# Optimization experiments

Hardware: AMD Instinct MI355X
Metric: run time of the kernel (lower is better)

## Reference

```python
import jax, jax.numpy as jnp
import numpy as np

H = 16  # num_heads

def setup_inputs() -> dict:
    key = jax.random.key(0)
    k1, k2, k3 = jax.random.split(key, 3)
    D = 1024
    x = jax.random.normal(k1, (4, 2048, D), dtype=jnp.float32)
    W_qkv = jax.random.normal(k2, (D, 3 * D), dtype=jnp.float32) * (1.0 / np.sqrt(D))
    b_qkv = jnp.zeros((3 * D,), dtype=jnp.float32)
    W_out = jax.random.normal(k3, (D, D), dtype=jnp.float32) * (1.0 / np.sqrt(D))
    b_out = jnp.zeros((D,), dtype=jnp.float32)
    return {"x": x, "W_qkv": W_qkv, "b_qkv": b_qkv, "W_out": W_out, "b_out": b_out}

def reference(x, W_qkv, b_qkv, W_out, b_out):
    B, S, D = x.shape
    hd = D // H  # head_dim
    qkv = x @ W_qkv + b_qkv  # [B,S,3D]
    q, k, v = jnp.split(qkv, 3, axis=-1)
    # [B,S,D] -> [B,H,S,hd]
    q = q.reshape(B, S, H, hd).transpose(0, 2, 1, 3)
    k = k.reshape(B, S, H, hd).transpose(0, 2, 1, 3)
    v = v.reshape(B, S, H, hd).transpose(0, 2, 1, 3)
    scores = jnp.einsum('bhqd,bhkd->bhqk', q, k) / jnp.sqrt(jnp.float32(hd))
    weights = jax.nn.softmax(scores, axis=-1)  # dropout p=0.0 (eval)
    out = jnp.einsum('bhqk,bhkd->bhqd', weights, v)
    out = out.transpose(0, 2, 1, 3).reshape(B, S, D)
    return out @ W_out + b_out
```

## Files before the change

### kernel.cpp

```cpp
#include <hip/hip_runtime.h>

typedef __bf16 bf16;
typedef __bf16 bf16x8 __attribute__((ext_vector_type(8)));
typedef float f32x4 __attribute__((ext_vector_type(4)));
typedef unsigned u32x2 __attribute__((ext_vector_type(2)));

static constexpr int NB = 4;
static constexpr int NS = 2048;
static constexpr int ND = 1024;
static constexpr int NH = 16;
static constexpr int HD = 64;
static constexpr float QSCALE = 0.18033688011112042f;

#define GL16(g, l)                                                             \
    __builtin_amdgcn_global_load_lds(                                          \
        (const __attribute__((address_space(1))) void*)(g),                    \
        (__attribute__((address_space(3))) void*)(l), 16, 0, 0)

static __device__ __forceinline__ unsigned pk2(float a, float b) {
    union { __bf16 h[2]; unsigned u; } t;
    t.h[0] = (__bf16)a; t.h[1] = (__bf16)b;
    return t.u;
}

__global__ void k_conv(const float* __restrict__ in, bf16* __restrict__ out, int n) {
    int i = (blockIdx.x * blockDim.x + threadIdx.x) * 4;
    if (i < n) {
        float4 v = *reinterpret_cast<const float4*>(in + i);
        bf16* o = out + i;
        o[0] = (bf16)v.x; o[1] = (bf16)v.y; o[2] = (bf16)v.z; o[3] = (bf16)v.w;
    }
}

__global__ void k_transconv(const float* __restrict__ in, bf16* __restrict__ out,
                            int K, int N) {
    __shared__ float tile[32][33];
    int k0 = blockIdx.y * 32, n0 = blockIdx.x * 32;
    int tx = threadIdx.x, ty = threadIdx.y;
    for (int j = 0; j < 32; j += 8)
        tile[ty + j][tx] = in[(long)(k0 + ty + j) * N + n0 + tx];
    __syncthreads();
    for (int j = 0; j < 32; j += 8)
        out[(long)(n0 + ty + j) * K + k0 + tx] = (bf16)tile[tx][ty + j];
}

template <int EPI>
__global__ __launch_bounds__(256, 2) void k_gemm(
    const bf16* __restrict__ A, const bf16* __restrict__ Bt,
    const float* __restrict__ bias,
    void* __restrict__ out0, void* __restrict__ out1, void* __restrict__ out2,
    int M, int N, int Kd)
{
    constexpr int BM = 128, BN = 128, BK = 64;
    __shared__ __align__(16) bf16 As[2][BM * BK];
    __shared__ __align__(16) bf16 Bs[2][BN * BK];

    const int t = threadIdx.x;
    const int wid = t >> 6, lane = t & 63;
    const int wm = wid >> 1, wn = wid & 1;
    const int m0 = blockIdx.y * BM, n0 = blockIdx.x * BN;
    const int lrow = lane & 15, lhi = lane >> 4;

    const int srow0 = wid * 32 + (lane >> 3);
    const int scol = ((lane & 7) ^ (lane >> 3)) * 8;
    const bf16* ag = A + (long)(m0 + srow0) * Kd + scol;
    const bf16* bg = Bt + (long)(n0 + srow0) * Kd + scol;

    auto STAGE = [&](int buf_, int k0_) {
#pragma unroll
        for (int c = 0; c < 4; ++c) {
            GL16(ag + (long)(c * 8) * Kd + k0_, &As[buf_][(wid * 32 + c * 8) * BK]);
            GL16(bg + (long)(c * 8) * Kd + k0_, &Bs[buf_][(wid * 32 + c * 8) * BK]);
        }
    };

    f32x4 acc[4][4] = {};
    const int nt = Kd >> 6;
    const int swzr = (lrow & 7) << 4;
    int co[2];
#pragma unroll
    for (int kk = 0; kk < 2; ++kk)
        co[kk] = ((kk * 64 + lhi * 16) ^ swzr) >> 1;

    STAGE(0, 0);
    __syncthreads();
    int cur = 0;
    for (int tix = 0; tix < nt; ++tix) {
        if (tix + 1 < nt) STAGE(cur ^ 1, (tix + 1) * BK);

        bf16x8 af[2][4], bfr[2][4];
#pragma unroll
        for (int kk = 0; kk < 2; ++kk)
#pragma unroll
            for (int i = 0; i < 4; ++i) {
                af[kk][i]  = *reinterpret_cast<const bf16x8*>(
                    &As[cur][(wm * 64 + i * 16 + lrow) * BK + co[kk]]);
                bfr[kk][i] = *reinterpret_cast<const bf16x8*>(
                    &Bs[cur][(wn * 64 + i * 16 + lrow) * BK + co[kk]]);
            }
        __builtin_amdgcn_s_setprio(1);
#pragma unroll
        for (int kk = 0; kk < 2; ++kk)
#pragma unroll
            for (int i = 0; i < 4; ++i)
#pragma unroll
                for (int j = 0; j < 4; ++j)
                    acc[i][j] = __builtin_amdgcn_mfma_f32_16x16x32_bf16(
                        af[kk][i], bfr[kk][j], acc[i][j], 0, 0, 0);
        __builtin_amdgcn_s_setprio(0);
        __syncthreads();
        cur ^= 1;
    }

    if (EPI == 0) {
        bf16* Qb = (bf16*)out0; bf16* Kb = (bf16*)out1; bf16* Vt = (bf16*)out2;
#pragma unroll
        for (int j = 0; j < 4; ++j) {
            int col = n0 + wn * 64 + j * 16 + lrow;
            float bv = bias[col];
            int which = col >> 10;
            int rem = col & 1023;
            int h = rem >> 6, d = rem & 63;
#pragma unroll
            for (int i = 0; i < 4; ++i) {
                int mbase = m0 + wm * 64 + i * 16 + lhi * 4;
#pragma unroll
                for (int r = 0; r < 4; ++r) {
                    int row = mbase + r;
                    int bb = row >> 11, s = row & 2047;
                    long bh = bb * NH + h;
                    float v = acc[i][j][r] + bv;
                    if (which == 0)      Qb[(bh * NS + s) * HD + d] = (bf16)(v * QSCALE);
                    else if (which == 1) Kb[(bh * NS + s) * HD + d] = (bf16)v;
                    else                 Vt[(bh * HD + d) * NS + s] = (bf16)v;
                }
            }
        }
    } else {
        float* O = (float*)out0;
#pragma unroll
        for (int j = 0; j < 4; ++j) {
            int col = n0 + wn * 64 + j * 16 + lrow;
            float bv = bias[col];
#pragma unroll
            for (int i = 0; i < 4; ++i) {
                int mbase = m0 + wm * 64 + i * 16 + lhi * 4;
#pragma unroll
                for (int r = 0; r < 4; ++r)
                    O[(long)(mbase + r) * N + col] = acc[i][j][r] + bv;
            }
        }
    }
}

__global__ __launch_bounds__(256, 4) void k_attn(
    const bf16* __restrict__ Qb, const bf16* __restrict__ Kb,
    const bf16* __restrict__ Vt, bf16* __restrict__ Ao)
{
    constexpr int KB = 64;
    constexpr int NT = NS / KB;
    __shared__ __align__(16) bf16 Ks[2][KB * HD];
    __shared__ __align__(16) bf16 Vs[2][HD * KB];
    __shared__ __align__(16) bf16 Ps[4 * 16 * 64];

    const int t = threadIdx.x;
    const int wid = t >> 6, lane = t & 63;
    const int lrow = lane & 15, lhi = lane >> 4;

    const int flat = blockIdx.y * gridDim.x + blockIdx.x;
    const int n = (flat & 7) * 128 + (flat >> 3);
    const int bh = n >> 4;
    const int qw = (n & 15) * 128 + wid * 32;

    const bf16* Qg = Qb + ((long)bh * NS + qw) * HD;
    const bf16* Kg = Kb + (long)bh * NS * HD;
    const bf16* Vg = Vt + (long)bh * HD * NS;

    bf16x8 qf[2][2];
#pragma unroll
    for (int qfr = 0; qfr < 2; ++qfr)
#pragma unroll
        for (int c = 0; c < 2; ++c)
            qf[qfr][c] = *reinterpret_cast<const bf16x8*>(
                Qg + (long)(qfr * 16 + lrow) * HD + c * 32 + lhi * 8);

    f32x4 of[2][4] = {};
    float lsum[2] = {0.f, 0.f};

    const int gsr = lane >> 3;
    const int gsc = ((lane & 7) ^ gsr) * 8;
    auto STAGE = [&](int buf, int kb) {
#pragma unroll
        for (int c = 0; c < 2; ++c) {
            const int rb = wid * 16 + c * 8;
            GL16(Kg + (long)(kb + rb + gsr) * HD + gsc, &Ks[buf][rb * 64]);
            GL16(Vg + (long)(rb + gsr) * NS + kb + gsc, &Vs[buf][rb * 64]);
        }
    };

    const int rsw = (lrow & 7) << 4;
    bf16* psw = &Ps[wid * 1024 + lrow * 64];

    auto COMPUTE = [&](int b_) {
        f32x4 st[2][4] = {};
        __builtin_amdgcn_s_setprio(1);
#pragma unroll
        for (int j = 0; j < 4; ++j)
#pragma unroll
            for (int c = 0; c < 2; ++c) {
                bf16x8 kf = *reinterpret_cast<const bf16x8*>(
                    &Ks[b_][(j * 16 + lrow) * 64 + (((c * 64 + lhi * 16) ^ rsw) >> 1)]);
#pragma unroll
                for (int qfr = 0; qfr < 2; ++qfr)
                    st[qfr][j] = __builtin_amdgcn_mfma_f32_16x16x32_bf16(
                        kf, qf[qfr][c], st[qfr][j], 0, 0, 0);
            }
        __builtin_amdgcn_s_setprio(0);

#pragma unroll
        for (int qfr = 0; qfr < 2; ++qfr) {
#pragma unroll
            for (int j = 0; j < 4; ++j) {
                float e0 = __builtin_amdgcn_exp2f(st[qfr][j][0]);
                float e1 = __builtin_amdgcn_exp2f(st[qfr][j][1]);
                float e2 = __builtin_amdgcn_exp2f(st[qfr][j][2]);
                float e3 = __builtin_amdgcn_exp2f(st[qfr][j][3]);
                lsum[qfr] += (e0 + e1) + (e2 + e3);
                u32x2 w; w[0] = pk2(e0, e1); w[1] = pk2(e2, e3);
                *reinterpret_cast<u32x2*>(
                    reinterpret_cast<char*>(psw) + (((j * 32 + lhi * 8) ^ rsw))) = w;
            }
            asm volatile("" ::: "memory");
#pragma unroll
            for (int chunk = 0; chunk < 2; ++chunk) {
                bf16x8 pf = *reinterpret_cast<const bf16x8*>(
                    reinterpret_cast<char*>(psw) + ((chunk * 64 + lhi * 16) ^ rsw));
                __builtin_amdgcn_s_setprio(1);
#pragma unroll
                for (int f = 0; f < 4; ++f) {
                    bf16x8 vf = *reinterpret_cast<const bf16x8*>(
                        &Vs[b_][(f * 16 + lrow) * 64 +
                                (((chunk * 64 + lhi * 16) ^ rsw) >> 1)]);
                    of[qfr][f] = __builtin_amdgcn_mfma_f32_16x16x32_bf16(
                        pf, vf, of[qfr][f], 0, 0, 0);
                }
                __builtin_amdgcn_s_setprio(0);
            }
            asm volatile("" ::: "memory");
        }
    };

    STAGE(0, 0);
    for (int it = 0; it < NT; it += 2) {
        __syncthreads();
        STAGE(1, (it + 1) * KB);
        COMPUTE(0);
        __syncthreads();
        if (it + 2 < NT) STAGE(0, (it + 2) * KB);
        COMPUTE(1);
    }

#pragma unroll
    for (int qfr = 0; qfr < 2; ++qfr) {
        lsum[qfr] += __shfl_xor(lsum[qfr], 16);
        lsum[qfr] += __shfl_xor(lsum[qfr], 32);
    }

    const int bb = bh >> 4, h = bh & 15;
#pragma unroll
    for (int qfr = 0; qfr < 2; ++qfr) {
#pragma unroll
        for (int r = 0; r < 4; ++r) {
            float inv = 1.0f / __shfl(lsum[qfr], 4 * lhi + r);
            int s = qw + qfr * 16 + 4 * lhi + r;
#pragma unroll
            for (int f = 0; f < 4; ++f)
                Ao[((long)bb * NS + s) * ND + h * HD + f * 16 + lrow] =
                    (bf16)(of[qfr][f][r] * inv);
        }
    }
}

extern "C" void kernel_launch(void* const* d_in, const int* in_sizes, int n_in,
                              void* d_out, int out_size, void* d_ws, size_t ws_size,
                              hipStream_t stream) {
    const float* x    = (const float*)d_in[0];
    const float* Wqkv = (const float*)d_in[1];
    const float* bqkv = (const float*)d_in[2];
    const float* Wout = (const float*)d_in[3];
    const float* bout = (const float*)d_in[4];
    float* out = (float*)d_out;

    char* ws = (char*)d_ws;
    bf16* Xb  = (bf16*)(ws);
    bf16* Wqt = (bf16*)(ws + 16777216);
    bf16* Wot = (bf16*)(ws + 23068672);
    bf16* Qb  = (bf16*)(ws + 25165824);
    bf16* Kb  = (bf16*)(ws + 41943040);
    bf16* Vt  = (bf16*)(ws + 58720256);
    bf16* Ab  = (bf16*)(ws + 75497472);

    k_conv<<<dim3(8192), dim3(256), 0, stream>>>(x, Xb, NB * NS * ND);
    k_transconv<<<dim3(96, 32), dim3(32, 8), 0, stream>>>(Wqkv, Wqt, ND, 3 * ND);
    k_transconv<<<dim3(32, 32), dim3(32, 8), 0, stream>>>(Wout, Wot, ND, ND);

    k_gemm<0><<<dim3(24, 64), dim3(256), 0, stream>>>(
        Xb, Wqt, bqkv, Qb, Kb, Vt, NB * NS, 3 * ND, ND);

    k_attn<<<dim3(16, 64), dim3(256), 0, stream>>>(Qb, Kb, Vt, Ab);

    k_gemm<1><<<dim3(8, 64), dim3(256), 0, stream>>>(
        Ab, Wot, bout, out, nullptr, nullptr, NB * NS, ND, ND);
}
```

Measured before the change: 221.5 us.

## Use explicit vmcnt waits and raw barriers; batch PV MFMAs across query fragments

Both the GEMM and attention loops replace __syncthreads with partial s_waitcnt vmcnt counts plus raw s_barrier. This lets the prefetch of the next tile stay in flight while only the current tile's loads are awaited. The attention PV step now loads both P fragments first, then reuses each V fragment across both query fragments, halving V LDS reads and giving longer MFMA chains. This relies on hand-counted outstanding load numbers, so it risks races if the compiler emits loads differently.

New measurement: 219.5 us. No clear change (-0.9%).

```diff
diff --git a/kernel.cpp b/kernel.cpp
--- a/kernel.cpp
+++ b/kernel.cpp
@@ -83,10 +83,16 @@
         co[kk] = ((kk * 64 + lhi * 16) ^ swzr) >> 1;
 
     STAGE(0, 0);
-    __syncthreads();
     int cur = 0;
     for (int tix = 0; tix < nt; ++tix) {
-        if (tix + 1 < nt) STAGE(cur ^ 1, (tix + 1) * BK);
+        if (tix + 1 < nt) {
+            STAGE(cur ^ 1, (tix + 1) * BK);
+            asm volatile("s_waitcnt vmcnt(8)" ::: "memory");
+        } else {
+            asm volatile("s_waitcnt vmcnt(0)" ::: "memory");
+        }
+        __builtin_amdgcn_s_barrier();
+        __builtin_amdgcn_sched_barrier(0);
 
         bf16x8 af[2][4], bfr[2][4];
 #pragma unroll
@@ -108,7 +114,7 @@
                     acc[i][j] = __builtin_amdgcn_mfma_f32_16x16x32_bf16(
                         af[kk][i], bfr[kk][j], acc[i][j], 0, 0, 0);
         __builtin_amdgcn_s_setprio(0);
-        __syncthreads();
+        __builtin_amdgcn_s_barrier();
         cur ^= 1;
     }
 
@@ -217,6 +223,7 @@
             }
         __builtin_amdgcn_s_setprio(0);
 
+        bf16x8 pfr[2][2];
 #pragma unroll
         for (int qfr = 0; qfr < 2; ++qfr) {
 #pragma unroll
@@ -232,32 +239,42 @@
             }
             asm volatile("" ::: "memory");
 #pragma unroll
-            for (int chunk = 0; chunk < 2; ++chunk) {
-                bf16x8 pf = *reinterpret_cast<const bf16x8*>(
+            for (int chunk = 0; chunk < 2; ++chunk)
+                pfr[qfr][chunk] = *reinterpret_cast<const bf16x8*>(
                     reinterpret_cast<char*>(psw) + ((chunk * 64 + lhi * 16) ^ rsw));
-                __builtin_amdgcn_s_setprio(1);
-#pragma unroll
-                for (int f = 0; f < 4; ++f) {
-                    bf16x8 vf = *reinterpret_cast<const bf16x8*>(
-                        &Vs[b_][(f * 16 + lrow) * 64 +
-                                (((chunk * 64 + lhi * 16) ^ rsw) >> 1)]);
+            asm volatile("" ::: "memory");
+        }
+
+        __builtin_amdgcn_s_setprio(1);
+#pragma unroll
+        for (int chunk = 0; chunk < 2; ++chunk)
+#pragma unroll
+            for (int f = 0; f < 4; ++f) {
+                bf16x8 vf = *reinterpret_cast<const bf16x8*>(
+                    &Vs[b_][(f * 16 + lrow) * 64 +
+                            (((chunk * 64 + lhi * 16) ^ rsw) >> 1)]);
+#pragma unroll
+                for (int qfr = 0; qfr < 2; ++qfr)
                     of[qfr][f] = __builtin_amdgcn_mfma_f32_16x16x32_bf16(
-                        pf, vf, of[qfr][f], 0, 0, 0);
-                }
-                __builtin_amdgcn_s_setprio(0);
-            }
-            asm volatile("" ::: "memory");
-        }
+                        pfr[qfr][chunk], vf, of[qfr][f], 0, 0, 0);
+            }
+        __builtin_amdgcn_s_setprio(0);
     };
 
     STAGE(0, 0);
-    for (int it = 0; it < NT; it += 2) {
-        __syncthreads();
-        STAGE(1, (it + 1) * KB);
-        COMPUTE(0);
-        __syncthreads();
-        if (it + 2 < NT) STAGE(0, (it + 2) * KB);
-        COMPUTE(1);
+    int cur = 0;
+    for (int it = 0; it < NT; ++it) {
+        if (it + 1 < NT) {
+            STAGE(cur ^ 1, (it + 1) * KB);
+            asm volatile("s_waitcnt vmcnt(4)" ::: "memory");
+        } else {
+            asm volatile("s_waitcnt vmcnt(0)" ::: "memory");
+        }
+        __builtin_amdgcn_s_barrier();
+        __builtin_amdgcn_sched_barrier(0);
+        COMPUTE(cur);
+        __builtin_amdgcn_s_barrier();
+        cur ^= 1;
     }
 
 #pragma unroll
```
